# Kernel tuning notes

Hardware: AMD Instinct MI355X
Metric: run time of the kernel (lower is better)

The kernel has to match this reference:

```python
import jax, jax.numpy as jnp
import numpy as np

N_HEAD = 16
MASK_VALUE = -10000.0


def setup_inputs() -> dict:
    key = jax.random.key(0)
    k1, k2, k3 = jax.random.split(key, 3)
    B, S, D = 2, 2048, 1024
    x = jax.random.normal(k1, (B, S, D), dtype=jnp.float32)
    W_qkv = jax.random.normal(k2, (D, 3 * D), dtype=jnp.float32) * 0.02
    b_qkv = jnp.zeros((3 * D,), dtype=jnp.float32)
    W_out = jax.random.normal(k3, (D, D), dtype=jnp.float32) * 0.02
    b_out = jnp.zeros((D,), dtype=jnp.float32)
    return {"x": x, "W_qkv": W_qkv, "b_qkv": b_qkv, "W_out": W_out, "b_out": b_out}


def reference(x, W_qkv, b_qkv, W_out, b_out):
    B, S, D = x.shape
    H = N_HEAD
    hd = D // H
    # fused QKV projection
    qkv = x @ W_qkv + b_qkv                      # [B, S, 3D]
    q, k, v = jnp.split(qkv, 3, axis=-1)
    # split heads -> [B, H, S, hd]
    def split_heads(t):
        return t.reshape(B, S, H, hd).transpose(0, 2, 1, 3)
    q, k, v = split_heads(q), split_heads(k), split_heads(v)
    # scaled causal attention with explicit mask-fill (matches ops.attention)
    scale = 1.0 / jnp.sqrt(jnp.asarray(hd, dtype=x.dtype))
    w = jnp.einsum('bhqd,bhkd->bhqk', q, k) * scale   # [B, H, S, S]
    causal = jnp.tril(jnp.ones((S, S), dtype=bool))    # [S, S]
    w = jnp.where(causal, w, jnp.asarray(MASK_VALUE, dtype=w.dtype))
    a = jax.nn.softmax(w, axis=-1)
    o = jnp.einsum('bhqk,bhkd->bhqd', a, v)            # [B, H, S, hd]
    # merge heads -> [B, S, D]
    o = o.transpose(0, 2, 1, 3).reshape(B, S, D)
    out = o @ W_out + b_out
    return out
```

## Files before the change

kernel.cpp:

```cpp
#include <hip/hip_runtime.h>
#include <hip/hip_bf16.h>
#include <stdint.h>

#define BATCH 2
#define SEQ   2048
#define DIM   1024
#define NH    16
#define HD    64
#define MVAL  (-10000.0f)

#if __has_builtin(__builtin_amdgcn_exp2f)
#define EXP2(x) __builtin_amdgcn_exp2f(x)
#define QSCALE  (0.125f * 1.44269504f)
#else
#define EXP2(x) __expf(x)
#define QSCALE  0.125f
#endif

typedef __attribute__((ext_vector_type(8))) short bf16x8;
typedef __attribute__((ext_vector_type(4))) float f32x4;
typedef __attribute__((ext_vector_type(16))) float f32x16;
typedef unsigned short u16;

static __device__ __forceinline__ u16 f2bf(float f) {
  union { float f; uint32_t u; } c; c.f = f;
  uint32_t x = c.u;
  return (u16)((x + 0x7fffu + ((x >> 16) & 1u)) >> 16);
}

static __device__ __forceinline__ uint32_t pk2(float a, float b) {
  __hip_bfloat162 h = __float22bfloat162_rn(make_float2(a, b));
  union { __hip_bfloat162 h; uint32_t u; } c; c.h = h;
  return c.u;
}

static __device__ __forceinline__ int swz128(int row, int chunk) {
  return row * 128 + (((chunk ^ (row & 7)) & 7) << 4);
}

static __device__ __forceinline__ void gload_lds16(const void* g, void* l) {
  __builtin_amdgcn_global_load_lds((const __attribute__((address_space(1))) void*)g,
                                   (__attribute__((address_space(3))) void*)l, 16, 0, 0);
}

__global__ void prep_kernel(const float* __restrict__ x, u16* __restrict__ xb,
                            const float* __restrict__ Wqkv, u16* __restrict__ WqkvT,
                            const float* __restrict__ Wout, u16* __restrict__ WoutT) {
  __shared__ float tile[32][33];
  int blk = blockIdx.x, tid = threadIdx.x;
  if (blk < 4096) {
    int i = blk * 256 + tid;
    float4 v = reinterpret_cast<const float4*>(x)[i];
    reinterpret_cast<uint2*>(xb)[i] = make_uint2(pk2(v.x, v.y), pk2(v.z, v.w));
    return;
  }
  const float* in;
  u16* out;
  int C, t;
  if (blk < 4096 + 3072) { t = blk - 4096; in = Wqkv; out = WqkvT; C = 3072; }
  else                   { t = blk - 7168; in = Wout; out = WoutT; C = 1024; }
  int R = DIM;
  int c0 = (t % (C / 32)) * 32, r0 = (t / (C / 32)) * 32;
  int tx = tid & 31, ty = tid >> 5;
#pragma unroll
  for (int i = 0; i < 32; i += 8)
    tile[ty + i][tx] = in[(size_t)(r0 + ty + i) * C + c0 + tx];
  __syncthreads();
#pragma unroll
  for (int i = 0; i < 32; i += 8)
    out[(size_t)(c0 + ty + i) * R + r0 + tx] = f2bf(tile[tx][ty + i]);
}

__global__ void vtrans_kernel(const u16* __restrict__ Vi, u16* __restrict__ Vo) {
  __shared__ __align__(16) char t[8192];
  int tid = threadIdx.x;
  int bh = blockIdx.y, s0 = blockIdx.x * 64;
  const u16* src = Vi + ((size_t)bh * SEQ + s0) * HD;
#pragma unroll
  for (int i = 0; i < 2; i++) {
    int r = i * 32 + (tid >> 3), ch = tid & 7;
    uint4 v = *reinterpret_cast<const uint4*>(src + (size_t)r * HD + ch * 8);
    *reinterpret_cast<uint4*>(t + swz128(r, ch)) = v;
  }
  __syncthreads();
  int d = tid >> 2, sc = tid & 3;
  u16 vals[16];
#pragma unroll
  for (int j = 0; j < 16; j++) {
    int s = sc * 16 + j;
    vals[j] = *reinterpret_cast<const u16*>(
        t + s * 128 + ((((d >> 3) ^ (s & 7)) & 7) << 4) + (d & 7) * 2);
  }
  u16* dst = Vo + ((size_t)bh * HD + d) * SEQ + s0 + sc * 16;
  *reinterpret_cast<uint4*>(dst) = *reinterpret_cast<const uint4*>(vals);
  *reinterpret_cast<uint4*>(dst + 8) = *reinterpret_cast<const uint4*>(vals + 8);
}

template <int EPI>
__global__ __launch_bounds__(256, 2) void gemm_bt_kernel(
    const u16* __restrict__ A, const u16* __restrict__ Bt,
    const float* __restrict__ bias, float* __restrict__ Cout,
    u16* __restrict__ Qo, u16* __restrict__ Ko, u16* __restrict__ Vo,
    int M, int N, int K) {
  __shared__ __align__(16) char lds[32768];
  char* As = lds;
  char* Bs = lds + 16384;
  int tid = threadIdx.x;
  int lane = tid & 63, l15 = lane & 15, l4 = lane >> 4;
  int w = tid >> 6, wr = w >> 1, wc = w & 1;
  int m0 = blockIdx.y * 128, n0 = blockIdx.x * 128;
  int srow = tid >> 3, sch = tid & 7;
  int sc_swz = ((sch ^ (srow & 7)) << 3);

  const u16* Ap = A + (size_t)(m0 + srow) * K + sc_swz;
  const u16* Bp = Bt + (size_t)(n0 + srow) * K + sc_swz;

  f32x4 acc[4][4] = {};

  for (int k0 = 0; k0 < K; k0 += 64) {
    __syncthreads();
#pragma unroll
    for (int i = 0; i < 4; i++) {
      gload_lds16(Ap + (size_t)i * 32 * K + k0, As + i * 4096 + tid * 16);
      gload_lds16(Bp + (size_t)i * 32 * K + k0, Bs + i * 4096 + tid * 16);
    }
    __syncthreads();
#pragma unroll
    for (int ks = 0; ks < 2; ks++) {
      int ch = ks * 4 + l4;
      bf16x8 af[4], bfv[4];
#pragma unroll
      for (int mi = 0; mi < 4; mi++)
        af[mi] = *reinterpret_cast<const bf16x8*>(As + swz128(wr * 64 + mi * 16 + l15, ch));
#pragma unroll
      for (int nj = 0; nj < 4; nj++)
        bfv[nj] = *reinterpret_cast<const bf16x8*>(Bs + swz128(wc * 64 + nj * 16 + l15, ch));
#pragma unroll
      for (int nj = 0; nj < 4; nj++)
#pragma unroll
        for (int mi = 0; mi < 4; mi++)
          acc[nj][mi] = __builtin_amdgcn_mfma_f32_16x16x32_bf16(bfv[nj], af[mi], acc[nj][mi], 0, 0, 0);
    }
  }

#pragma unroll
  for (int nj = 0; nj < 4; nj++) {
    int nb = n0 + wc * 64 + nj * 16 + l4 * 4;
    float4 bv = *reinterpret_cast<const float4*>(bias + nb);
#pragma unroll
    for (int mi = 0; mi < 4; mi++) {
      int m = m0 + wr * 64 + mi * 16 + l15;
      f32x4 a = acc[nj][mi];
      float v0 = a[0] + bv.x, v1 = a[1] + bv.y, v2 = a[2] + bv.z, v3 = a[3] + bv.w;
      if (EPI == 1) {
        *reinterpret_cast<float4*>(Cout + (size_t)m * N + nb) = make_float4(v0, v1, v2, v3);
      } else {
        int b = m >> 11, s = m & 2047;
        int sec = nb >> 10, c = nb & 1023, h = c >> 6, d = c & 63;
        size_t bh = (size_t)(b * NH + h);
        u16* dst;
        float scl;
        if (sec == 0)      { dst = Qo; scl = QSCALE; }
        else if (sec == 1) { dst = Ko; scl = 1.0f; }
        else               { dst = Vo; scl = 1.0f; }
        *reinterpret_cast<uint2*>(dst + (bh * SEQ + s) * HD + d) =
            make_uint2(pk2(v0 * scl, v1 * scl), pk2(v2 * scl, v3 * scl));
      }
    }
  }
}

__global__ __launch_bounds__(256, 2) void attn_kernel(
    const u16* __restrict__ Q, const u16* __restrict__ K,
    const u16* __restrict__ Vt, u16* __restrict__ O) {
  __shared__ __align__(16) char lds[65536];
  int tid = threadIdx.x, lane = tid & 63, w = tid >> 6;
  int l31 = lane & 31, hi = lane >> 5;
  int sub = w & 1, par = w >> 1;
  int blk = blockIdx.x;
  int bh = (blk & 7) * 4 + ((blk >> 3) & 3);
  int p = blk >> 5;
  const u16* Qh = Q + (size_t)bh * SEQ * HD;
  const u16* Kh = K + (size_t)bh * SEQ * HD;
  const u16* Vh = Vt + (size_t)bh * HD * SEQ;
  int srow = tid >> 3, sch = tid & 7;
  int b_ = bh >> 4, h_ = bh & 15;

  auto stageKV = [&](int b, int T) {
    const u16* Kt = Kh + (size_t)T * 128 * HD;
    const u16* Vs = Vh + (size_t)T * 128;
    char* Kb = lds + b * 16384;
    char* Vb = lds + 32768 + b * 16384;
#pragma unroll
    for (int i = 0; i < 4; i++) {
      int row = i * 32 + srow;
      int c = (sch ^ (row & 7)) << 3;
      gload_lds16(Kt + (size_t)row * HD + c, Kb + row * 128 + sch * 16);
    }
#pragma unroll
    for (int sv = 0; sv < 2; sv++)
#pragma unroll
      for (int i = 0; i < 2; i++) {
        int d = i * 32 + srow;
        int c = (sch ^ (d & 7)) << 3;
        gload_lds16(Vs + (size_t)d * SEQ + sv * 64 + c, Vb + sv * 8192 + d * 128 + sch * 16);
      }
  };

  int buf = 0;
  stageKV(0, 0);
  __syncthreads();

  for (int pass = 0; pass < 2; pass++) {
    int qt = (pass == 0) ? (31 - p) : p;
    int nT = (qt + 2) >> 1;
    int qb = qt * 64 + sub * 32;

    bf16x8 qf[4];
#pragma unroll
    for (int ks = 0; ks < 4; ks++)
      qf[ks] = *reinterpret_cast<const bf16x8*>(
          Qh + (size_t)(qb + l31) * HD + ks * 16 + hi * 8);

    float mrun = -1e30f, lrun = 0.0f;
    f32x16 oacc[2] = {};
    bf16x8 pf_c[4], vf_c[2][4];
    bool pend = false;

    for (int T = 0; T < nT; T++) {
      int nxt = (T + 1 < nT) ? (T + 1) : (pass == 0 ? 0 : -1);
      if (nxt >= 0) stageKV(buf ^ 1, nxt);

      char* Kw = lds + buf * 16384 + par * 8192;
      char* Vw = lds + 32768 + buf * 16384 + par * 8192;
      int kvb = T * 128 + par * 64;

      __builtin_amdgcn_s_setprio(1);
      if (pend) {
#pragma unroll
        for (int ks = 0; ks < 4; ks++)
#pragma unroll
          for (int nd = 0; nd < 2; nd++)
            oacc[nd] = __builtin_amdgcn_mfma_f32_32x32x16_bf16(
                vf_c[nd][ks], pf_c[ks], oacc[nd], 0, 0, 0);
      }

      f32x16 s[2] = {};
#pragma unroll
      for (int ks = 0; ks < 4; ks++)
#pragma unroll
        for (int n = 0; n < 2; n++) {
          bf16x8 kf = *reinterpret_cast<const bf16x8*>(
              Kw + swz128(n * 32 + l31, 2 * ks + hi));
          s[n] = __builtin_amdgcn_mfma_f32_32x32x16_bf16(kf, qf[ks], s[n], 0, 0, 0);
        }
      __builtin_amdgcn_s_setprio(0);

#pragma unroll
      for (int nd = 0; nd < 2; nd++)
#pragma unroll
        for (int ks = 0; ks < 4; ks++)
          vf_c[nd][ks] = *reinterpret_cast<const bf16x8*>(
              Vw + swz128(nd * 32 + l31, 2 * ks + hi));

      if (kvb + 63 > qb) {
        int qg = qb + l31;
#pragma unroll
        for (int n = 0; n < 2; n++)
#pragma unroll
          for (int r = 0; r < 16; r++) {
            int kg = kvb + n * 32 + (r & 3) + 8 * (r >> 2) + 4 * hi;
            if (kg > qg) s[n][r] = MVAL;
          }
      }

      float mt = s[0][0];
#pragma unroll
      for (int n = 0; n < 2; n++)
#pragma unroll
        for (int r = 0; r < 16; r++) mt = fmaxf(mt, s[n][r]);
      mt = fmaxf(mt, __shfl_xor(mt, 32));

      if (!__all(mt <= mrun)) {
        float mnew = fmaxf(mrun, mt);
        float alpha = EXP2(mrun - mnew);
        mrun = mnew;
#pragma unroll
        for (int nd = 0; nd < 2; nd++)
#pragma unroll
          for (int r = 0; r < 16; r++) oacc[nd][r] *= alpha;
        lrun *= alpha;
      }

      float rs = 0.0f;
#pragma unroll
      for (int n = 0; n < 2; n++)
#pragma unroll
        for (int r = 0; r < 16; r++) {
          float pv = EXP2(s[n][r] - mrun);
          s[n][r] = pv;
          rs += pv;
        }
      rs += __shfl_xor(rs, 32);
      lrun += rs;

#pragma unroll
      for (int n = 0; n < 2; n++)
#pragma unroll
        for (int half = 0; half < 2; half++) {
          int rb = half * 8;
          uint32_t a0 = pk2(s[n][rb + 0], s[n][rb + 1]);
          uint32_t b0 = pk2(s[n][rb + 4], s[n][rb + 5]);
          asm("v_permlane32_swap_b32 %0, %1" : "+v"(a0), "+v"(b0));
          uint32_t a1 = pk2(s[n][rb + 2], s[n][rb + 3]);
          uint32_t b1 = pk2(s[n][rb + 6], s[n][rb + 7]);
          asm("v_permlane32_swap_b32 %0, %1" : "+v"(a1), "+v"(b1));
          union { uint32_t u[4]; bf16x8 v; } bw;
          bw.u[0] = a0; bw.u[1] = a1; bw.u[2] = b0; bw.u[3] = b1;
          pf_c[n * 2 + half] = bw.v;
        }
      pend = true;

      __syncthreads();
      buf ^= 1;
    }

    __builtin_amdgcn_s_setprio(1);
#pragma unroll
    for (int ks = 0; ks < 4; ks++)
#pragma unroll
      for (int nd = 0; nd < 2; nd++)
        oacc[nd] = __builtin_amdgcn_mfma_f32_32x32x16_bf16(
            vf_c[nd][ks], pf_c[ks], oacc[nd], 0, 0, 0);
    __builtin_amdgcn_s_setprio(0);

    char* Xo = lds + (buf ^ 1) * 16384;
    float* Xml = (float*)(lds + 32768 + (buf ^ 1) * 16384);
    int row = sub * 32 + l31;
    if (par == 1) {
      if (hi == 0) {
        Xml[row * 2] = mrun;
        Xml[row * 2 + 1] = lrun;
      }
#pragma unroll
      for (int nd = 0; nd < 2; nd++)
#pragma unroll
        for (int g = 0; g < 4; g++) {
          int chunk = 8 * nd + 2 * g + hi;
          f32x4 t;
          t[0] = oacc[nd][4 * g];     t[1] = oacc[nd][4 * g + 1];
          t[2] = oacc[nd][4 * g + 2]; t[3] = oacc[nd][4 * g + 3];
          *reinterpret_cast<f32x4*>(Xo + row * 256 + (((chunk ^ (row & 7)) & 15) << 4)) = t;
        }
    }
    __syncthreads();
    if (par == 0) {
      float mB = Xml[row * 2], lB = Xml[row * 2 + 1];
      float m = fmaxf(mrun, mB);
      float wA = EXP2(mrun - m), wB = EXP2(mB - m);
      float linv = 1.0f / (lrun * wA + lB * wB);
      float fA = wA * linv, fB = wB * linv;
      u16* orow = O + ((size_t)b_ * SEQ + qb + l31) * DIM + h_ * HD;
#pragma unroll
      for (int nd = 0; nd < 2; nd++)
#pragma unroll
        for (int g = 0; g < 4; g++) {
          int chunk = 8 * nd + 2 * g + hi;
          f32x4 ob = *reinterpret_cast<const f32x4*>(
              Xo + row * 256 + (((chunk ^ (row & 7)) & 15) << 4));
          float o0 = oacc[nd][4 * g] * fA + ob[0] * fB;
          float o1 = oacc[nd][4 * g + 1] * fA + ob[1] * fB;
          float o2 = oacc[nd][4 * g + 2] * fA + ob[2] * fB;
          float o3 = oacc[nd][4 * g + 3] * fA + ob[3] * fB;
          int d0 = nd * 32 + 8 * g + 4 * hi;
          *reinterpret_cast<uint2*>(orow + d0) = make_uint2(pk2(o0, o1), pk2(o2, o3));
        }
    }
    __syncthreads();
  }
}

extern "C" void kernel_launch(void* const* d_in, const int* in_sizes, int n_in,
                              void* d_out, int out_size, void* d_ws, size_t ws_size,
                              hipStream_t stream) {
  const float* x     = (const float*)d_in[0];
  const float* W_qkv = (const float*)d_in[1];
  const float* b_qkv = (const float*)d_in[2];
  const float* W_out = (const float*)d_in[3];
  const float* b_out = (const float*)d_in[4];
  float* out = (float*)d_out;
  char* ws = (char*)d_ws;

  u16* xb    = (u16*)(ws);
  u16* WqkvT = (u16*)(ws + 8388608);
  u16* WoutT = (u16*)(ws + 8388608 + 6291456);
  u16* Qb    = (u16*)(ws + 16777216);
  u16* Kb    = (u16*)(ws + 16777216 + 8388608);
  u16* Vtb   = (u16*)(ws + 16777216 + 2 * 8388608);
  u16* Ob    = (u16*)(ws + 16777216 + 3 * 8388608);
  u16* Vraw  = Ob;

  prep_kernel<<<4096 + 3072 + 1024, 256, 0, stream>>>(x, xb, W_qkv, WqkvT, W_out, WoutT);
  gemm_bt_kernel<0><<<dim3(3 * DIM / 128, BATCH * SEQ / 128), 256, 0, stream>>>(
      xb, WqkvT, b_qkv, nullptr, Qb, Kb, Vraw, BATCH * SEQ, 3 * DIM, DIM);
  vtrans_kernel<<<dim3(SEQ / 64, BATCH * NH), 256, 0, stream>>>(Vraw, Vtb);
  attn_kernel<<<512, 256, 0, stream>>>(Qb, Kb, Vtb, Ob);
  gemm_bt_kernel<1><<<dim3(DIM / 128, BATCH * SEQ / 128), 256, 0, stream>>>(
      Ob, WoutT, b_out, out, nullptr, nullptr, nullptr, BATCH * SEQ, DIM, DIM);
}
```

Before: 116.2 us.

## Split attention KV range across four waves per 32-row query tile

Each block now handles a single 32-row query tile, and its four waves take interleaved 64-key tiles, each wave staging its own K into private LDS buffers with no block-wide barrier per iteration. V fragments are read directly from global memory instead of through LDS, and the grid doubles to 1024 blocks. The four partial softmax states are merged through LDS at the end. The aim is to remove per-tile __syncthreads and improve parallelism and balance, at the cost of uncoalesced global V loads and a four-way merge.

```diff
diff --git a/kernel.cpp b/kernel.cpp
--- a/kernel.cpp
+++ b/kernel.cpp
@@ -176,45 +176,32 @@
   __shared__ __align__(16) char lds[65536];
   int tid = threadIdx.x, lane = tid & 63, w = tid >> 6;
   int l31 = lane & 31, hi = lane >> 5;
-  int sub = w & 1, par = w >> 1;
+  int par = w;
   int blk = blockIdx.x;
   int bh = (blk & 7) * 4 + ((blk >> 3) & 3);
   int p = blk >> 5;
   const u16* Qh = Q + (size_t)bh * SEQ * HD;
   const u16* Kh = K + (size_t)bh * SEQ * HD;
   const u16* Vh = Vt + (size_t)bh * HD * SEQ;
-  int srow = tid >> 3, sch = tid & 7;
+  char* myK = lds + w * 16384;
   int b_ = bh >> 4, h_ = bh & 15;
-
-  auto stageKV = [&](int b, int T) {
-    const u16* Kt = Kh + (size_t)T * 128 * HD;
-    const u16* Vs = Vh + (size_t)T * 128;
-    char* Kb = lds + b * 16384;
-    char* Vb = lds + 32768 + b * 16384;
-#pragma unroll
-    for (int i = 0; i < 4; i++) {
-      int row = i * 32 + srow;
-      int c = (sch ^ (row & 7)) << 3;
-      gload_lds16(Kt + (size_t)row * HD + c, Kb + row * 128 + sch * 16);
-    }
-#pragma unroll
-    for (int sv = 0; sv < 2; sv++)
-#pragma unroll
-      for (int i = 0; i < 2; i++) {
-        int d = i * 32 + srow;
-        int c = (sch ^ (d & 7)) << 3;
-        gload_lds16(Vs + (size_t)d * SEQ + sv * 64 + c, Vb + sv * 8192 + d * 128 + sch * 16);
-      }
+  int sr = lane >> 3, sc = lane & 7;
+
+  auto stageK = [&](int b, int T) {
+    const u16* Kt = Kh + (size_t)T * 64 * HD;
+    char* Kb = myK + b * 8192;
+#pragma unroll
+    for (int i = 0; i < 8; i++) {
+      int row = i * 8 + sr;
+      int cch = (sc ^ sr) << 3;
+      gload_lds16(Kt + (size_t)row * HD + cch, Kb + i * 1024 + lane * 16);
+    }
   };
 
-  int buf = 0;
-  stageKV(0, 0);
-  __syncthreads();
-
   for (int pass = 0; pass < 2; pass++) {
-    int qt = (pass == 0) ? (31 - p) : p;
-    int nT = (qt + 2) >> 1;
-    int qb = qt * 64 + sub * 32;
+    int c = pass ? p : (63 - p);
+    int nkt = (c + 2) >> 1;
+    int qb = c * 32;
 
     bf16x8 qf[4];
 #pragma unroll
@@ -226,14 +213,14 @@
     f32x16 oacc[2] = {};
     bf16x8 pf_c[4], vf_c[2][4];
     bool pend = false;
-
-    for (int T = 0; T < nT; T++) {
-      int nxt = (T + 1 < nT) ? (T + 1) : (pass == 0 ? 0 : -1);
-      if (nxt >= 0) stageKV(buf ^ 1, nxt);
-
-      char* Kw = lds + buf * 16384 + par * 8192;
-      char* Vw = lds + 32768 + buf * 16384 + par * 8192;
-      int kvb = T * 128 + par * 64;
+    int buf = 0;
+
+    if (par < nkt) stageK(0, par);
+
+    for (int T = par; T < nkt; T += 4) {
+      asm volatile("s_waitcnt vmcnt(0)" ::: "memory");
+      __builtin_amdgcn_sched_barrier(0);
+      if (T + 4 < nkt) stageK(buf ^ 1, T + 4);
 
       __builtin_amdgcn_s_setprio(1);
       if (pend) {
@@ -245,6 +232,7 @@
                 vf_c[nd][ks], pf_c[ks], oacc[nd], 0, 0, 0);
       }
 
+      char* Kw = myK + buf * 8192;
       f32x16 s[2] = {};
 #pragma unroll
       for (int ks = 0; ks < 4; ks++)
@@ -256,12 +244,14 @@
         }
       __builtin_amdgcn_s_setprio(0);
 
+      int kvb = T * 64;
+      const u16* Vs = Vh + kvb;
 #pragma unroll
       for (int nd = 0; nd < 2; nd++)
 #pragma unroll
         for (int ks = 0; ks < 4; ks++)
           vf_c[nd][ks] = *reinterpret_cast<const bf16x8*>(
-              Vw + swz128(nd * 32 + l31, 2 * ks + hi));
+              Vs + (size_t)(nd * 32 + l31) * SEQ + (2 * ks + hi) * 8);
 
       if (kvb + 63 > qb) {
         int qg = qb + l31;
@@ -320,27 +310,26 @@
           pf_c[n * 2 + half] = bw.v;
         }
       pend = true;
-
-      __syncthreads();
       buf ^= 1;
     }
 
-    __builtin_amdgcn_s_setprio(1);
-#pragma unroll
-    for (int ks = 0; ks < 4; ks++)
-#pragma unroll
-      for (int nd = 0; nd < 2; nd++)
-        oacc[nd] = __builtin_amdgcn_mfma_f32_32x32x16_bf16(
-            vf_c[nd][ks], pf_c[ks], oacc[nd], 0, 0, 0);
-    __builtin_amdgcn_s_setprio(0);
-
-    char* Xo = lds + (buf ^ 1) * 16384;
-    float* Xml = (float*)(lds + 32768 + (buf ^ 1) * 16384);
-    int row = sub * 32 + l31;
-    if (par == 1) {
+    if (pend) {
+      __builtin_amdgcn_s_setprio(1);
+#pragma unroll
+      for (int ks = 0; ks < 4; ks++)
+#pragma unroll
+        for (int nd = 0; nd < 2; nd++)
+          oacc[nd] = __builtin_amdgcn_mfma_f32_32x32x16_bf16(
+              vf_c[nd][ks], pf_c[ks], oacc[nd], 0, 0, 0);
+      __builtin_amdgcn_s_setprio(0);
+    }
+
+    int row = l31;
+    if (par != 0) {
       if (hi == 0) {
-        Xml[row * 2] = mrun;
-        Xml[row * 2 + 1] = lrun;
+        float* ml = (float*)(myK + 8192);
+        ml[row * 2] = mrun;
+        ml[row * 2 + 1] = lrun;
       }
 #pragma unroll
       for (int nd = 0; nd < 2; nd++)
@@ -350,30 +339,46 @@
           f32x4 t;
           t[0] = oacc[nd][4 * g];     t[1] = oacc[nd][4 * g + 1];
           t[2] = oacc[nd][4 * g + 2]; t[3] = oacc[nd][4 * g + 3];
-          *reinterpret_cast<f32x4*>(Xo + row * 256 + (((chunk ^ (row & 7)) & 15) << 4)) = t;
+          *reinterpret_cast<f32x4*>(myK + row * 256 + (((chunk ^ (row & 7)) & 15) << 4)) = t;
         }
     }
     __syncthreads();
     if (par == 0) {
-      float mB = Xml[row * 2], lB = Xml[row * 2 + 1];
-      float m = fmaxf(mrun, mB);
-      float wA = EXP2(mrun - m), wB = EXP2(mB - m);
-      float linv = 1.0f / (lrun * wA + lB * wB);
-      float fA = wA * linv, fB = wB * linv;
+      float mK[3], lK[3];
+      float mAll = mrun;
+#pragma unroll
+      for (int k = 0; k < 3; k++) {
+        float* ml = (float*)(lds + (k + 1) * 16384 + 8192);
+        mK[k] = ml[row * 2];
+        lK[k] = ml[row * 2 + 1];
+        mAll = fmaxf(mAll, mK[k]);
+      }
+      float wS = EXP2(mrun - mAll);
+      float lT = lrun * wS;
+      float wK[3];
+#pragma unroll
+      for (int k = 0; k < 3; k++) { wK[k] = EXP2(mK[k] - mAll); lT += lK[k] * wK[k]; }
+      float linv = 1.0f / lT;
       u16* orow = O + ((size_t)b_ * SEQ + qb + l31) * DIM + h_ * HD;
 #pragma unroll
       for (int nd = 0; nd < 2; nd++)
 #pragma unroll
         for (int g = 0; g < 4; g++) {
           int chunk = 8 * nd + 2 * g + hi;
-          f32x4 ob = *reinterpret_cast<const f32x4*>(
-              Xo + row * 256 + (((chunk ^ (row & 7)) & 15) << 4));
-          float o0 = oacc[nd][4 * g] * fA + ob[0] * fB;
-          float o1 = oacc[nd][4 * g + 1] * fA + ob[1] * fB;
-          float o2 = oacc[nd][4 * g + 2] * fA + ob[2] * fB;
-          float o3 = oacc[nd][4 * g + 3] * fA + ob[3] * fB;
+          int off = row * 256 + (((chunk ^ (row & 7)) & 15) << 4);
+          float o0 = oacc[nd][4 * g] * wS;
+          float o1 = oacc[nd][4 * g + 1] * wS;
+          float o2 = oacc[nd][4 * g + 2] * wS;
+          float o3 = oacc[nd][4 * g + 3] * wS;
+#pragma unroll
+          for (int k = 0; k < 3; k++) {
+            f32x4 ob = *reinterpret_cast<const f32x4*>(lds + (k + 1) * 16384 + off);
+            o0 += ob[0] * wK[k]; o1 += ob[1] * wK[k];
+            o2 += ob[2] * wK[k]; o3 += ob[3] * wK[k];
+          }
           int d0 = nd * 32 + 8 * g + 4 * hi;
-          *reinterpret_cast<uint2*>(orow + d0) = make_uint2(pk2(o0, o1), pk2(o2, o3));
+          *reinterpret_cast<uint2*>(orow + d0) =
+              make_uint2(pk2(o0 * linv, o1 * linv), pk2(o2 * linv, o3 * linv));
         }
     }
     __syncthreads();
@@ -404,7 +409,7 @@
   gemm_bt_kernel<0><<<dim3(3 * DIM / 128, BATCH * SEQ / 128), 256, 0, stream>>>(
       xb, WqkvT, b_qkv, nullptr, Qb, Kb, Vraw, BATCH * SEQ, 3 * DIM, DIM);
   vtrans_kernel<<<dim3(SEQ / 64, BATCH * NH), 256, 0, stream>>>(Vraw, Vtb);
-  attn_kernel<<<512, 256, 0, stream>>>(Qb, Kb, Vtb, Ob);
+  attn_kernel<<<1024, 256, 0, stream>>>(Qb, Kb, Vtb, Ob);
   gemm_bt_kernel<1><<<dim3(DIM / 128, BATCH * SEQ / 128), 256, 0, stream>>>(
       Ob, WoutT, b_out, out, nullptr, nullptr, nullptr, BATCH * SEQ, DIM, DIM);
 }
```

After: 130.9 us. +12.6%, slower.
